# Kernel optimization log

Hardware: AMD Instinct MI355X
Metric: run time of the kernel (lower is better)

The kernel has to match this reference:

```python
import jax, jax.numpy as jnp
import numpy as np

NS, NV = 48, 10                    # scalar / vector multiplicities (cfg.ns, cfg.nv)
WN = NS * NS + NS * NV             # per-edge TP weight numel: paths 0e*0e->0e and 0e*1o->1o
OUT = NS + 3 * NV                  # out irreps 48x0e + 10x1o -> 78 dims
INV = float(1.0 / np.sqrt(NS))     # e3nn-style path normalization (fan_in = mul_in)
N_LIG, N_REC, N_ATOM = 2000, 2000, 15000
E_LL, E_RR, E_AA = 15000, 10000, 15000
E_LR, E_LA, E_AR = 5000, 8000, 8000


def setup_inputs() -> dict:
    key = jax.random.key(0)
    ks = jax.random.split(key, 40)
    f = lambda i, shape, s=1.0: jax.random.normal(ks[i], shape, dtype=jnp.float32) * s
    ii = lambda i, n, e: jax.random.randint(ks[i], (e,), 0, n, dtype=jnp.int32)
    w_s = (1.0 / (3 * NS)) ** 0.5
    return {
        'lig_x': f(0, (N_LIG, NS)), 'rec_x': f(1, (N_REC, NS)), 'atom_x': f(2, (N_ATOM, NS)),
        'll_attr': f(3, (E_LL, NS)), 'rr_attr': f(4, (E_RR, NS)), 'aa_attr': f(5, (E_AA, NS)),
        'lr_attr': f(6, (E_LR, NS)), 'la_attr': f(7, (E_LA, NS)), 'ar_attr': f(8, (E_AR, NS)),
        'll_sh': f(9, (E_LL, 9)), 'rr_sh': f(10, (E_RR, 9)), 'aa_sh': f(11, (E_AA, 9)),
        'lr_sh': f(12, (E_LR, 9)), 'la_sh': f(13, (E_LA, 9)), 'ar_sh': f(14, (E_AR, 9)),
        'mlp_w1': f(15, (9, 3 * NS, 3 * NS), w_s), 'mlp_b1': jnp.zeros((9, 3 * NS), jnp.float32),
        'mlp_w2': f(16, (9, 3 * NS, 3 * NS), w_s), 'mlp_b2': jnp.zeros((9, 3 * NS), jnp.float32),
        'mlp_w3': f(17, (9, 3 * NS, WN), w_s), 'mlp_b3': jnp.zeros((9, WN), jnp.float32),
        'll_src': ii(18, N_LIG, E_LL), 'll_dst': ii(19, N_LIG, E_LL),
        'rr_src': ii(20, N_REC, E_RR), 'rr_dst': ii(21, N_REC, E_RR),
        'aa_src': ii(22, N_ATOM, E_AA), 'aa_dst': ii(23, N_ATOM, E_AA),
        'lr_lig': ii(24, N_LIG, E_LR), 'lr_rec': ii(25, N_REC, E_LR),
        'la_lig': ii(26, N_LIG, E_LA), 'la_atom': ii(27, N_ATOM, E_LA),
        'ar_atom': ii(28, N_ATOM, E_AR), 'ar_rec': ii(29, N_REC, E_AR),
    }


def _tp_conv(src_x, dst_x, e_attr, e_sh, src_idx, dst_idx, n_dst, w1, b1, w2, b2, w3, b3):
    """FullyConnectedTensorProductConv: per-edge MLP -> TP weights, CG tensor
    product of gathered source features with edge SH, mean scatter to dst."""
    fs = src_x[src_idx]                                          # (E, ns) gather
    z = jnp.concatenate([e_attr, fs, dst_x[dst_idx]], axis=-1)
    h = jax.nn.relu(z @ w1 + b1)
    h = jax.nn.relu(h @ w2 + b2)
    w = h @ w3 + b3                                              # (E, WN) edge-conditioned TP weights
    w0 = w[:, : NS * NS].reshape(-1, NS, NS)                     # 0e x 0e -> 0e path
    wv = w[:, NS * NS :].reshape(-1, NS, NV)                     # 0e x 1o -> 1o path
    out0 = jnp.einsum('ei,eio->eo', fs, w0) * e_sh[:, :1] * INV  # (E, ns)
    outv = jnp.einsum('ei,eiv,em->evm', fs, wv, e_sh[:, 1:4]) * INV  # (E, nv, 3)
    msg = jnp.concatenate([out0, outv.reshape(-1, NV * 3)], axis=-1)
    agg = jax.ops.segment_sum(msg, dst_idx, num_segments=n_dst)
    deg = jax.ops.segment_sum(jnp.ones((msg.shape[0], 1), msg.dtype), dst_idx, num_segments=n_dst)
    return agg / jnp.maximum(deg, 1.0)                           # mean reduction


def reference(lig_x, rec_x, atom_x, ll_attr, rr_attr, aa_attr, lr_attr, la_attr, ar_attr,
              ll_sh, rr_sh, aa_sh, lr_sh, la_sh, ar_sh,
              mlp_w1, mlp_b1, mlp_w2, mlp_b2, mlp_w3, mlp_b3,
              ll_src, ll_dst, rr_src, rr_dst, aa_src, aa_dst,
              lr_lig, lr_rec, la_lig, la_atom, ar_atom, ar_rec):
    P = lambda c: (mlp_w1[c], mlp_b1[c], mlp_w2[c], mlp_b2[c], mlp_w3[c], mlp_b3[c])
    # one interaction layer = 9 structurally distinct convs (lig/rec/atom intra + 6 cross dirs)
    lig_u = (_tp_conv(lig_x, lig_x, ll_attr, ll_sh, ll_src, ll_dst, N_LIG, *P(0))
           + _tp_conv(rec_x, lig_x, lr_attr, lr_sh, lr_rec, lr_lig, N_LIG, *P(1))
           + _tp_conv(atom_x, lig_x, la_attr, la_sh, la_atom, la_lig, N_LIG, *P(2)))
    rec_u = (_tp_conv(lig_x, rec_x, lr_attr, lr_sh, lr_lig, lr_rec, N_REC, *P(3))
           + _tp_conv(rec_x, rec_x, rr_attr, rr_sh, rr_src, rr_dst, N_REC, *P(4))
           + _tp_conv(atom_x, rec_x, ar_attr, ar_sh, ar_atom, ar_rec, N_REC, *P(5)))
    atom_u = (_tp_conv(lig_x, atom_x, la_attr, la_sh, la_lig, la_atom, N_ATOM, *P(6))
            + _tp_conv(rec_x, atom_x, ar_attr, ar_sh, ar_rec, ar_atom, N_ATOM, *P(7))
            + _tp_conv(atom_x, atom_x, aa_attr, aa_sh, aa_src, aa_dst, N_ATOM, *P(8)))
    pad = lambda x: jnp.pad(x, ((0, 0), (0, OUT - NS)))          # residual: pad scalars to out irreps
    return jnp.concatenate([pad(lig_x) + lig_u, pad(rec_x) + rec_u, pad(atom_x) + atom_u], axis=0)
```

## Files before the change

kernel.cpp:

```cpp
#include <hip/hip_runtime.h>


namespace {

constexpr int NCONV = 9;
constexpr int ETOT  = 82000;
constexpr float INV = 0.14433756729740643f;

constexpr int EC[NCONV]     = {15000,5000,8000,5000,10000,8000,8000,8000,15000};
constexpr int NBLKC[NCONV]  = {118,40,63,40,79,63,63,63,118};
constexpr int EOFF[NCONV]   = {0,15000,20000,28000,33000,43000,51000,59000,67000};
constexpr int DEGOFF[NCONV] = {0,2000,4000,6000,8000,10000,12000,27000,42000};
constexpr int NODEC[NCONV]  = {2000,2000,2000,2000,2000,2000,15000,15000,15000};
constexpr int NBLK_TOT = 647;

typedef _Float16 f16;
typedef __attribute__((ext_vector_type(8))) _Float16 f16x8;
typedef __attribute__((ext_vector_type(4))) _Float16 f16x4;
typedef __attribute__((ext_vector_type(4))) float f32x4;

#define MFMA(a, b, c) __builtin_amdgcn_mfma_f32_16x16x32_f16((a), (b), (c), 0, 0, 0)

struct ConvPtrs {
  const float* src_x[NCONV];
  const float* dst_x[NCONV];
  const float* attr[NCONV];
  const float* sh[NCONV];
  const int*   sidx[NCONV];
  const int*   didx[NCONV];
};

}

__device__ __forceinline__ int xcd_remap(int bid) {
  const int xcd = bid & 7, slot = bid >> 3;
  return (xcd <= 6) ? (xcd * 81 + slot) : (567 + slot);
}

__device__ __forceinline__ int conv_decode(int bid, int& rem) {
  int c = 0; rem = bid;
  while (c < NCONV - 1 && rem >= NBLKC[c]) { rem -= NBLKC[c]; ++c; }
  return c;
}

__device__ __forceinline__ void gld_lds16(const void* g, void* l) {
  __builtin_amdgcn_global_load_lds(
      (const __attribute__((address_space(1))) void*)g,
      (__attribute__((address_space(3))) void*)l, 16, 0, 0);
}

__device__ __forceinline__ f32x4 cvt4(f16x4 h) {
  return (f32x4){(float)h[0], (float)h[1], (float)h[2], (float)h[3]};
}

__global__ __launch_bounds__(64) void prep_w12(
    const float* __restrict__ w1, const float* __restrict__ b1,
    const float* __restrict__ w2, const float* __restrict__ b2,
    f16* __restrict__ w1f, f16* __restrict__ w2f) {
  const int b = blockIdx.x;
  const int sel = b >= 405, bb = sel ? b - 405 : b;
  const int c = bb / 45, r2 = bb % 45, cb = r2 / 5, s = r2 % 5;
  const float* w  = sel ? w2 : w1;
  const float* bi = sel ? b2 : b1;
  f16* dst = (sel ? w2f : w1f) + ((size_t)(c * 9 + cb) * 5 + s) * 512;
  const int l = threadIdx.x;
  const int n = cb * 16 + (l & 15);
  f16x8 pack;
#pragma unroll
  for (int j = 0; j < 8; ++j) {
    const int k = s * 32 + ((l >> 4) << 3) + j;
    float v = 0.f;
    if (k < 144)       v = w[((size_t)c * 144 + k) * 144 + n];
    else if (k == 144) v = bi[c * 144 + n];
    pack[j] = (f16)v;
  }
  ((f16x8*)dst)[l] = pack;
}

__global__ __launch_bounds__(256) void prep_w3k(
    const float* __restrict__ w3, const float* __restrict__ b3,
    f16* __restrict__ w3f) {
  const int b = blockIdx.x;
  const int c = b / 48, i = b % 48;
  const float* wc = w3 + (size_t)c * 144 * 2784;
  const float* bc = b3 + (size_t)c * 2784;
  f16* dst = w3f + (size_t)(c * 48 + i) * 20 * 512;
#pragma unroll 1
  for (int it = 0; it < 40; ++it) {
    const int f = it * 256 + threadIdx.x;
    const int s = f >> 11, g2 = f & 2047, cb = g2 >> 9, l = (g2 >> 3) & 63, j = f & 7;
    const int k = s * 32 + ((l >> 4) << 3) + j;
    const int col = cb * 16 + (l & 15);
    float v = 0.f;
    if (k <= 144) {
      const float* src = (k == 144) ? bc : (wc + (size_t)k * 2784);
      if (col < 48)      v = src[i * 48 + col];
      else if (col < 58) v = src[2304 + i * 10 + (col - 48)];
    }
    dst[f] = (f16)v;
  }
}

__global__ __launch_bounds__(256) void deg_kernel(ConvPtrs P, float* __restrict__ deg) {
  const int gid = blockIdx.x * 256 + threadIdx.x;
  if (gid >= ETOT) return;
  int c = 0;
  while (c < NCONV - 1 && gid >= EOFF[c + 1]) ++c;
  const int e = gid - EOFF[c];
  atomicAdd(&deg[DEGOFF[c] + P.didx[c][e]], 1.0f);
}

__global__ __launch_bounds__(256) void scan_kernel(
    const float* __restrict__ deg, int* __restrict__ offs, int* __restrict__ cursor) {
  __shared__ int part[256];
  const int c = blockIdx.x, N = NODEC[c], base = DEGOFF[c];
  const int tid = threadIdx.x;
  const int chunk = (N + 255) / 256;
  const int start = tid * chunk;
  const int end = (start + chunk < N) ? (start + chunk) : N;
  int s = 0;
  for (int i = start; i < end; ++i) s += (int)deg[base + i];
  part[tid] = s;
  __syncthreads();
  if (tid == 0) {
    int acc = 0;
    for (int k = 0; k < 256; ++k) { int t = part[k]; part[k] = acc; acc += t; }
  }
  __syncthreads();
  int acc = part[tid];
  for (int i = start; i < end; ++i) {
    offs[base + i] = acc; cursor[base + i] = acc;
    acc += (int)deg[base + i];
  }
}

__global__ __launch_bounds__(256) void slot_kernel(
    ConvPtrs P, int* __restrict__ cursor, int* __restrict__ eslot) {
  const int gid = blockIdx.x * 256 + threadIdx.x;
  if (gid >= ETOT) return;
  int c = 0;
  while (c < NCONV - 1 && gid >= EOFF[c + 1]) ++c;
  const int e = gid - EOFF[c];
  const int d = P.didx[c][e];
  const int pos = atomicAdd(&cursor[DEGOFF[c] + d], 1);
  eslot[EOFF[c] + pos] = e;
}

template<int NCB, int CB0>
__device__ __forceinline__ void layer_mm(
    const f16x8* __restrict__ Av, const f16x8* __restrict__ wv,
    int c, int lane, int wr, f32x4 acc[4][5]) {
#pragma unroll
  for (int rb = 0; rb < 4; ++rb)
#pragma unroll
    for (int cb = 0; cb < NCB; ++cb) acc[rb][cb] = (f32x4)0.0f;
#pragma unroll
  for (int s = 0; s < 5; ++s) {
    f16x8 B[NCB];
#pragma unroll
    for (int cb = 0; cb < NCB; ++cb)
      B[cb] = wv[((size_t)(c * 9 + CB0 + cb) * 5 + s) * 64 + lane];
    f16x8 A[4];
#pragma unroll
    for (int rb = 0; rb < 4; ++rb) A[rb] = Av[((wr * 4 + rb) * 5 + s) * 64 + lane];
#pragma unroll
    for (int rb = 0; rb < 4; ++rb)
#pragma unroll
      for (int cb = 0; cb < NCB; ++cb)
        acc[rb][cb] = MFMA(A[rb], B[cb], acc[rb][cb]);
  }
}

template<int NCB, int CB0>
__device__ __forceinline__ void layer_wb(const f32x4 acc[4][5], f16* __restrict__ At,
                                         int lane, int wr) {
#pragma unroll
  for (int cb = 0; cb < NCB; ++cb) {
    const int k = (CB0 + cb) * 16 + (lane & 15);
    const int s = k >> 5, g = (k >> 3) & 3, j = k & 7;
#pragma unroll
    for (int rb = 0; rb < 4; ++rb)
#pragma unroll
      for (int r = 0; r < 4; ++r) {
        const int row = ((lane >> 4) << 2) + r;
        At[((((wr * 4 + rb) * 5 + s) * 4 + g) * 16 + row) * 8 + j] =
            (f16)fmaxf(acc[rb][cb][r], 0.f);
      }
  }
}

__global__ __launch_bounds__(256, 3) void fused_conv(
    ConvPtrs P, const f16* __restrict__ w1f, const f16* __restrict__ w2f,
    const f16* __restrict__ w3f, float* __restrict__ medge) {
  __shared__ __align__(16) char smem[54272];
  f16* Atile = (f16*)smem;
  f16 (*fst)[128] = (f16 (*)[128])(smem + 40960);
  int* sidb = (int*)(smem + 53248);
  int* dstb = (int*)(smem + 53760);

  int rem; const int c = conv_decode(xcd_remap(blockIdx.x), rem);
  const int E = EC[c], e0 = rem * 128;
  const int tid = threadIdx.x, lane = tid & 63, w = tid >> 6;
  const int wr = w >> 1, wc = w & 1;

  if (tid < 128) {
    int ec = e0 + tid; if (ec >= E) ec = E - 1;
    sidb[tid] = P.sidx[c][ec];
    dstb[tid] = P.didx[c][ec];
  }
  __syncthreads();

  {
    const float* attr = P.attr[c];
    const float* sx = P.src_x[c];
    const float* dx = P.dst_x[c];
#pragma unroll 1
    for (int it = 0; it < 10; ++it) {
      const int u = it * 256 + tid, j8 = u >> 7, e = u & 127;
      int ec = e0 + e; if (ec >= E) ec = E - 1;
      float v[8];
      if (j8 < 6) {
        const float* p = attr + (size_t)ec * 48 + j8 * 8;
#pragma unroll
        for (int t = 0; t < 8; ++t) v[t] = p[t];
      } else if (j8 < 12) {
        const float* p = sx + (size_t)sidb[e] * 48 + (j8 - 6) * 8;
#pragma unroll
        for (int t = 0; t < 8; ++t) v[t] = p[t];
#pragma unroll
        for (int t = 0; t < 8; ++t) fst[(j8 - 6) * 8 + t][e] = (f16)v[t];
      } else if (j8 < 18) {
        const float* p = dx + (size_t)dstb[e] * 48 + (j8 - 12) * 8;
#pragma unroll
        for (int t = 0; t < 8; ++t) v[t] = p[t];
      } else if (j8 == 18) {
        v[0] = 1.f;
#pragma unroll
        for (int t = 1; t < 8; ++t) v[t] = 0.f;
      } else {
#pragma unroll
        for (int t = 0; t < 8; ++t) v[t] = 0.f;
      }
      f16x8 h;
#pragma unroll
      for (int t = 0; t < 8; ++t) h[t] = (f16)v[t];
      const int s = j8 >> 2, g = j8 & 3, rbg = e >> 4, row = e & 15;
      ((f16x8*)Atile)[((rbg * 5 + s) * 4 + g) * 16 + row] = h;
    }
  }
  __syncthreads();

  const f16x8* Av = (const f16x8*)Atile;

  f32x4 acc[4][5];
  if (wc == 0) layer_mm<5, 0>(Av, (const f16x8*)w1f, c, lane, wr, acc);
  else         layer_mm<4, 5>(Av, (const f16x8*)w1f, c, lane, wr, acc);
  __syncthreads();
  if (wc == 0) layer_wb<5, 0>(acc, Atile, lane, wr);
  else         layer_wb<4, 5>(acc, Atile, lane, wr);
  __syncthreads();
  if (wc == 0) layer_mm<5, 0>(Av, (const f16x8*)w2f, c, lane, wr, acc);
  else         layer_mm<4, 5>(Av, (const f16x8*)w2f, c, lane, wr, acc);
  __syncthreads();
  if (wc == 0) layer_wb<5, 0>(acc, Atile, lane, wr);
  else         layer_wb<4, 5>(acc, Atile, lane, wr);
  __syncthreads();

  f16x8 Af[4][5];
#pragma unroll
  for (int rb = 0; rb < 4; ++rb)
#pragma unroll
    for (int s = 0; s < 5; ++s)
      Af[rb][s] = Av[((wr * 4 + rb) * 5 + s) * 64 + lane];
  __syncthreads();

  const f16* __restrict__ w3c = w3f + (size_t)(c * 48) * 10240;
  f16* buf0 = Atile;
  f16* buf1 = Atile + 10240;

  f32x4 msg[4][2];
#pragma unroll
  for (int rb = 0; rb < 4; ++rb)
#pragma unroll
    for (int cb = 0; cb < 2; ++cb) msg[rb][cb] = (f32x4)0.0f;

#pragma unroll
  for (int q = 0; q < 5; ++q) {
    const int chunk = q * 4 + w;
    gld_lds16(w3c + chunk * 512 + lane * 8, buf0 + chunk * 512);
  }
  __syncthreads();

#pragma unroll 1
  for (int i = 0; i < 48; ++i) {
    f16* bcur = (i & 1) ? buf1 : buf0;
    f16* bnxt = (i & 1) ? buf0 : buf1;
    if (i + 1 < 48) {
      const f16* gsrc = w3c + (size_t)(i + 1) * 10240;
#pragma unroll
      for (int q = 0; q < 5; ++q) {
        const int chunk = q * 4 + w;
        gld_lds16(gsrc + chunk * 512 + lane * 8, bnxt + chunk * 512);
      }
    }
    f16x4 fsh[4];
#pragma unroll
    for (int rb = 0; rb < 4; ++rb)
      fsh[rb] = *(const f16x4*)&fst[i][wr * 64 + rb * 16 + ((lane >> 4) << 2)];

    const f16x8* bv = (const f16x8*)bcur;
#pragma unroll
    for (int cb = 0; cb < 2; ++cb) {
      f16x8 Bf[5];
#pragma unroll
      for (int s = 0; s < 5; ++s) Bf[s] = bv[(s * 4 + wc * 2 + cb) * 64 + lane];
      f32x4 T[4];
#pragma unroll
      for (int rb = 0; rb < 4; ++rb) T[rb] = (f32x4)0.0f;
#pragma unroll
      for (int s = 0; s < 5; ++s)
#pragma unroll
        for (int rb = 0; rb < 4; ++rb) T[rb] = MFMA(Af[rb][s], Bf[s], T[rb]);
#pragma unroll
      for (int rb = 0; rb < 4; ++rb) msg[rb][cb] += cvt4(fsh[rb]) * T[rb];
    }
    __syncthreads();
  }

  const float* __restrict__ shp = P.sh[c];
#pragma unroll
  for (int rb = 0; rb < 4; ++rb)
#pragma unroll
    for (int r = 0; r < 4; ++r) {
      const int el = wr * 64 + rb * 16 + ((lane >> 4) << 2) + r;
      const int ec = e0 + el;
      if (ec >= E) continue;
      const size_t ge = (size_t)(EOFF[c] + ec);
      const float* shq = shp + (size_t)ec * 9;
      const float s0 = shq[0], s1 = shq[1], s2 = shq[2], s3 = shq[3];
      float* mp = medge + ge * 80;
#pragma unroll
      for (int cb = 0; cb < 2; ++cb) {
        const int col = (wc * 2 + cb) * 16 + (lane & 15);
        const float v = msg[rb][cb][r] * INV;
        if (col < 48) {
          mp[col] = v * s0;
        } else if (col < 58) {
          const int vv = col - 48;
          mp[48 + vv * 3 + 0] = v * s1;
          mp[48 + vv * 3 + 1] = v * s2;
          mp[48 + vv * 3 + 2] = v * s3;
        }
      }
    }
}

__global__ __launch_bounds__(256) void finalize_kernel(
    const float* __restrict__ lig, const float* __restrict__ rec,
    const float* __restrict__ atom, const float* __restrict__ deg,
    const int* __restrict__ offs, const int* __restrict__ eslot,
    const float* __restrict__ medge, float* __restrict__ out) {
  const int half = threadIdx.x >> 7;
  const int j = threadIdx.x & 127;
  const int row = blockIdx.x * 2 + half;
  if (row >= 19000 || j >= 78) return;
  int node, cb; const float* x;
  if (row < 2000)      { node = row;        cb = 0; x = lig; }
  else if (row < 4000) { node = row - 2000; cb = 3; x = rec; }
  else                 { node = row - 4000; cb = 6; x = atom; }
  float r = (j < 48) ? x[(size_t)node * 48 + j] : 0.f;
#pragma unroll
  for (int t = 0; t < 3; ++t) {
    const int c = cb + t;
    const int base = DEGOFF[c] + node;
    const float d = deg[base];
    const int n = (int)d;
    const int o = offs[base];
    float s = 0.f;
    for (int k = 0; k < n; ++k) {
      const int e = eslot[EOFF[c] + o + k];
      s += medge[(size_t)(EOFF[c] + e) * 80 + j];
    }
    r += s * (1.f / fmaxf(d, 1.f));
  }
  out[(size_t)row * 78 + j] = r;
}

extern "C" void kernel_launch(void* const* d_in, const int* in_sizes, int n_in,
                              void* d_out, int out_size, void* d_ws, size_t ws_size,
                              hipStream_t stream) {
  (void)in_sizes; (void)n_in; (void)out_size; (void)ws_size;
  const float* lig_x  = (const float*)d_in[0];
  const float* rec_x  = (const float*)d_in[1];
  const float* atom_x = (const float*)d_in[2];
  const float* attr_ll = (const float*)d_in[3];
  const float* attr_rr = (const float*)d_in[4];
  const float* attr_aa = (const float*)d_in[5];
  const float* attr_lr = (const float*)d_in[6];
  const float* attr_la = (const float*)d_in[7];
  const float* attr_ar = (const float*)d_in[8];
  const float* sh_ll = (const float*)d_in[9];
  const float* sh_rr = (const float*)d_in[10];
  const float* sh_aa = (const float*)d_in[11];
  const float* sh_lr = (const float*)d_in[12];
  const float* sh_la = (const float*)d_in[13];
  const float* sh_ar = (const float*)d_in[14];
  const float* w1 = (const float*)d_in[15];
  const float* b1 = (const float*)d_in[16];
  const float* w2 = (const float*)d_in[17];
  const float* b2 = (const float*)d_in[18];
  const float* w3 = (const float*)d_in[19];
  const float* b3 = (const float*)d_in[20];
  const int* ll_src = (const int*)d_in[21];
  const int* ll_dst = (const int*)d_in[22];
  const int* rr_src = (const int*)d_in[23];
  const int* rr_dst = (const int*)d_in[24];
  const int* aa_src = (const int*)d_in[25];
  const int* aa_dst = (const int*)d_in[26];
  const int* lr_lig = (const int*)d_in[27];
  const int* lr_rec = (const int*)d_in[28];
  const int* la_lig = (const int*)d_in[29];
  const int* la_atom = (const int*)d_in[30];
  const int* ar_atom = (const int*)d_in[31];
  const int* ar_rec  = (const int*)d_in[32];

  f16* w1f = (f16*)d_ws;
  f16* w2f = w1f + 207360;
  f16* w3f = w2f + 207360;
  float* deg   = (float*)(w3f + 4423680);
  int*   offs  = (int*)(deg + 57000);
  int*   cursor= offs + 57000;
  int*   eslot = cursor + 57000;
  float* medge = (float*)(eslot + 82000);

  ConvPtrs P;
  const float* SX[NCONV] = {lig_x, rec_x, atom_x, lig_x, rec_x, atom_x, lig_x, rec_x, atom_x};
  const float* DX[NCONV] = {lig_x, lig_x, lig_x, rec_x, rec_x, rec_x, atom_x, atom_x, atom_x};
  const float* AT[NCONV] = {attr_ll, attr_lr, attr_la, attr_lr, attr_rr, attr_ar, attr_la, attr_ar, attr_aa};
  const float* SH[NCONV] = {sh_ll, sh_lr, sh_la, sh_lr, sh_rr, sh_ar, sh_la, sh_ar, sh_aa};
  const int*   SI[NCONV] = {ll_src, lr_rec, la_atom, lr_lig, rr_src, ar_atom, la_lig, ar_rec, aa_src};
  const int*   DI[NCONV] = {ll_dst, lr_lig, la_lig, lr_rec, rr_dst, ar_rec, la_atom, ar_atom, aa_dst};
  for (int cc = 0; cc < NCONV; ++cc) {
    P.src_x[cc] = SX[cc]; P.dst_x[cc] = DX[cc]; P.attr[cc] = AT[cc];
    P.sh[cc] = SH[cc]; P.sidx[cc] = SI[cc]; P.didx[cc] = DI[cc];
  }

  prep_w12<<<810, 64, 0, stream>>>(w1, b1, w2, b2, w1f, w2f);
  prep_w3k<<<432, 256, 0, stream>>>(w3, b3, w3f);
  hipMemsetAsync(deg, 0, 57000 * sizeof(float), stream);
  deg_kernel<<<(ETOT + 255) / 256, 256, 0, stream>>>(P, deg);
  scan_kernel<<<NCONV, 256, 0, stream>>>(deg, offs, cursor);
  slot_kernel<<<(ETOT + 255) / 256, 256, 0, stream>>>(P, cursor, eslot);
  fused_conv<<<NBLK_TOT, 256, 0, stream>>>(P, w1f, w2f, w3f, medge);
  finalize_kernel<<<9500, 256, 0, stream>>>(lig_x, rec_x, atom_x, deg, offs,
                                            eslot, medge, (float*)d_out);
}
```

Baseline: 231.9 us.

## Write edge messages in CSR slot order and merge prep kernels

The three weight-prep kernels and the degree count are merged into one launch. The slot kernel now records each edge's CSR position, and fused_conv writes pre-scaled messages (including the 1/deg mean) straight into that sorted slot. Finalize then reads each node's messages as one contiguous range with no indirection, and each block handles 3 rows of 80 threads. This removes the eslot gather and one launch, at the cost of scattered writes in fused_conv and a deg lookup per edge.

```diff
diff --git a/kernel.cpp b/kernel.cpp
--- a/kernel.cpp
+++ b/kernel.cpp
@@ -53,61 +53,62 @@
   return (f32x4){(float)h[0], (float)h[1], (float)h[2], (float)h[3]};
 }
 
-__global__ __launch_bounds__(64) void prep_w12(
+__global__ __launch_bounds__(256) void prep_all(
+    ConvPtrs P,
     const float* __restrict__ w1, const float* __restrict__ b1,
     const float* __restrict__ w2, const float* __restrict__ b2,
-    f16* __restrict__ w1f, f16* __restrict__ w2f) {
-  const int b = blockIdx.x;
-  const int sel = b >= 405, bb = sel ? b - 405 : b;
-  const int c = bb / 45, r2 = bb % 45, cb = r2 / 5, s = r2 % 5;
-  const float* w  = sel ? w2 : w1;
-  const float* bi = sel ? b2 : b1;
-  f16* dst = (sel ? w2f : w1f) + ((size_t)(c * 9 + cb) * 5 + s) * 512;
-  const int l = threadIdx.x;
-  const int n = cb * 16 + (l & 15);
-  f16x8 pack;
-#pragma unroll
-  for (int j = 0; j < 8; ++j) {
-    const int k = s * 32 + ((l >> 4) << 3) + j;
-    float v = 0.f;
-    if (k < 144)       v = w[((size_t)c * 144 + k) * 144 + n];
-    else if (k == 144) v = bi[c * 144 + n];
-    pack[j] = (f16)v;
-  }
-  ((f16x8*)dst)[l] = pack;
-}
-
-__global__ __launch_bounds__(256) void prep_w3k(
     const float* __restrict__ w3, const float* __restrict__ b3,
-    f16* __restrict__ w3f) {
-  const int b = blockIdx.x;
-  const int c = b / 48, i = b % 48;
-  const float* wc = w3 + (size_t)c * 144 * 2784;
-  const float* bc = b3 + (size_t)c * 2784;
-  f16* dst = w3f + (size_t)(c * 48 + i) * 20 * 512;
+    f16* __restrict__ w1f, f16* __restrict__ w2f, f16* __restrict__ w3f,
+    float* __restrict__ deg) {
+  const int blk = blockIdx.x;
+  if (blk < 203) {
+    const int unit = blk * 4 + (threadIdx.x >> 6);
+    if (unit >= 810) return;
+    const int l = threadIdx.x & 63;
+    const int sel = unit >= 405, bb = sel ? unit - 405 : unit;
+    const int c = bb / 45, r2 = bb % 45, cb = r2 / 5, s = r2 % 5;
+    const float* w  = sel ? w2 : w1;
+    const float* bi = sel ? b2 : b1;
+    f16* dst = (sel ? w2f : w1f) + ((size_t)(c * 9 + cb) * 5 + s) * 512;
+    const int n = cb * 16 + (l & 15);
+    f16x8 pack;
+#pragma unroll
+    for (int j = 0; j < 8; ++j) {
+      const int k = s * 32 + ((l >> 4) << 3) + j;
+      float v = 0.f;
+      if (k < 144)       v = w[((size_t)c * 144 + k) * 144 + n];
+      else if (k == 144) v = bi[c * 144 + n];
+      pack[j] = (f16)v;
+    }
+    ((f16x8*)dst)[l] = pack;
+  } else if (blk < 635) {
+    const int b = blk - 203;
+    const int c = b / 48, i = b % 48;
+    const float* wc = w3 + (size_t)c * 144 * 2784;
+    const float* bc = b3 + (size_t)c * 2784;
+    f16* dst = w3f + (size_t)(c * 48 + i) * 20 * 512;
 #pragma unroll 1
-  for (int it = 0; it < 40; ++it) {
-    const int f = it * 256 + threadIdx.x;
-    const int s = f >> 11, g2 = f & 2047, cb = g2 >> 9, l = (g2 >> 3) & 63, j = f & 7;
-    const int k = s * 32 + ((l >> 4) << 3) + j;
-    const int col = cb * 16 + (l & 15);
-    float v = 0.f;
-    if (k <= 144) {
-      const float* src = (k == 144) ? bc : (wc + (size_t)k * 2784);
-      if (col < 48)      v = src[i * 48 + col];
-      else if (col < 58) v = src[2304 + i * 10 + (col - 48)];
-    }
-    dst[f] = (f16)v;
-  }
-}
-
-__global__ __launch_bounds__(256) void deg_kernel(ConvPtrs P, float* __restrict__ deg) {
-  const int gid = blockIdx.x * 256 + threadIdx.x;
-  if (gid >= ETOT) return;
-  int c = 0;
-  while (c < NCONV - 1 && gid >= EOFF[c + 1]) ++c;
-  const int e = gid - EOFF[c];
-  atomicAdd(&deg[DEGOFF[c] + P.didx[c][e]], 1.0f);
+    for (int it = 0; it < 40; ++it) {
+      const int f = it * 256 + threadIdx.x;
+      const int s = f >> 11, g2 = f & 2047, cb = g2 >> 9, l = (g2 >> 3) & 63, j = f & 7;
+      const int k = s * 32 + ((l >> 4) << 3) + j;
+      const int col = cb * 16 + (l & 15);
+      float v = 0.f;
+      if (k <= 144) {
+        const float* src = (k == 144) ? bc : (wc + (size_t)k * 2784);
+        if (col < 48)      v = src[i * 48 + col];
+        else if (col < 58) v = src[2304 + i * 10 + (col - 48)];
+      }
+      dst[f] = (f16)v;
+    }
+  } else {
+    const int gid = (blk - 635) * 256 + threadIdx.x;
+    if (gid >= ETOT) return;
+    int c = 0;
+    while (c < NCONV - 1 && gid >= EOFF[c + 1]) ++c;
+    const int e = gid - EOFF[c];
+    atomicAdd(&deg[DEGOFF[c] + P.didx[c][e]], 1.0f);
+  }
 }
 
 __global__ __launch_bounds__(256) void scan_kernel(
@@ -135,15 +136,14 @@
 }
 
 __global__ __launch_bounds__(256) void slot_kernel(
-    ConvPtrs P, int* __restrict__ cursor, int* __restrict__ eslot) {
+    ConvPtrs P, int* __restrict__ cursor, int* __restrict__ inv_slot) {
   const int gid = blockIdx.x * 256 + threadIdx.x;
   if (gid >= ETOT) return;
   int c = 0;
   while (c < NCONV - 1 && gid >= EOFF[c + 1]) ++c;
   const int e = gid - EOFF[c];
   const int d = P.didx[c][e];
-  const int pos = atomicAdd(&cursor[DEGOFF[c] + d], 1);
-  eslot[EOFF[c] + pos] = e;
+  inv_slot[gid] = atomicAdd(&cursor[DEGOFF[c] + d], 1);
 }
 
 template<int NCB, int CB0>
@@ -191,7 +191,8 @@
 
 __global__ __launch_bounds__(256, 3) void fused_conv(
     ConvPtrs P, const f16* __restrict__ w1f, const f16* __restrict__ w2f,
-    const f16* __restrict__ w3f, float* __restrict__ medge) {
+    const f16* __restrict__ w3f, const float* __restrict__ deg,
+    const int* __restrict__ inv_slot, float* __restrict__ medge) {
   __shared__ __align__(16) char smem[54272];
   f16* Atile = (f16*)smem;
   f16 (*fst)[128] = (f16 (*)[128])(smem + 40960);
@@ -328,6 +329,7 @@
   }
 
   const float* __restrict__ shp = P.sh[c];
+  const float* __restrict__ degc = deg + DEGOFF[c];
 #pragma unroll
   for (int rb = 0; rb < 4; ++rb)
 #pragma unroll
@@ -335,14 +337,16 @@
       const int el = wr * 64 + rb * 16 + ((lane >> 4) << 2) + r;
       const int ec = e0 + el;
       if (ec >= E) continue;
-      const size_t ge = (size_t)(EOFF[c] + ec);
+      const int dst = dstb[el];
+      const float sc = INV / fmaxf(degc[dst], 1.f);
       const float* shq = shp + (size_t)ec * 9;
       const float s0 = shq[0], s1 = shq[1], s2 = shq[2], s3 = shq[3];
-      float* mp = medge + ge * 80;
+      const int pos = inv_slot[EOFF[c] + ec];
+      float* mp = medge + (size_t)(EOFF[c] + pos) * 80;
 #pragma unroll
       for (int cb = 0; cb < 2; ++cb) {
         const int col = (wc * 2 + cb) * 16 + (lane & 15);
-        const float v = msg[rb][cb][r] * INV;
+        const float v = msg[rb][cb][r] * sc;
         if (col < 48) {
           mp[col] = v * s0;
         } else if (col < 58) {
@@ -357,12 +361,13 @@
 
 __global__ __launch_bounds__(256) void finalize_kernel(
     const float* __restrict__ lig, const float* __restrict__ rec,
-    const float* __restrict__ atom, const float* __restrict__ deg,
-    const int* __restrict__ offs, const int* __restrict__ eslot,
-    const float* __restrict__ medge, float* __restrict__ out) {
-  const int half = threadIdx.x >> 7;
-  const int j = threadIdx.x & 127;
-  const int row = blockIdx.x * 2 + half;
+    const float* __restrict__ atom, const int* __restrict__ offs,
+    const int* __restrict__ cursor, const float* __restrict__ medge,
+    float* __restrict__ out) {
+  const int tid = threadIdx.x;
+  if (tid >= 240) return;
+  const int r3 = tid / 80, j = tid - r3 * 80;
+  const int row = blockIdx.x * 3 + r3;
   if (row >= 19000 || j >= 78) return;
   int node, cb; const float* x;
   if (row < 2000)      { node = row;        cb = 0; x = lig; }
@@ -373,15 +378,9 @@
   for (int t = 0; t < 3; ++t) {
     const int c = cb + t;
     const int base = DEGOFF[c] + node;
-    const float d = deg[base];
-    const int n = (int)d;
-    const int o = offs[base];
-    float s = 0.f;
-    for (int k = 0; k < n; ++k) {
-      const int e = eslot[EOFF[c] + o + k];
-      s += medge[(size_t)(EOFF[c] + e) * 80 + j];
-    }
-    r += s * (1.f / fmaxf(d, 1.f));
+    const int o = offs[base], e = cursor[base];
+    for (int k = o; k < e; ++k)
+      r += medge[(size_t)(EOFF[c] + k) * 80 + j];
   }
   out[(size_t)row * 78 + j] = r;
 }
@@ -427,11 +426,11 @@
   f16* w1f = (f16*)d_ws;
   f16* w2f = w1f + 207360;
   f16* w3f = w2f + 207360;
-  float* deg   = (float*)(w3f + 4423680);
-  int*   offs  = (int*)(deg + 57000);
-  int*   cursor= offs + 57000;
-  int*   eslot = cursor + 57000;
-  float* medge = (float*)(eslot + 82000);
+  float* deg     = (float*)(w3f + 4423680);
+  int*   offs    = (int*)(deg + 57000);
+  int*   cursor  = offs + 57000;
+  int*   inv_slot= cursor + 57000;
+  float* medge   = (float*)(inv_slot + 82000);
 
   ConvPtrs P;
   const float* SX[NCONV] = {lig_x, rec_x, atom_x, lig_x, rec_x, atom_x, lig_x, rec_x, atom_x};
@@ -445,13 +444,11 @@
     P.sh[cc] = SH[cc]; P.sidx[cc] = SI[cc]; P.didx[cc] = DI[cc];
   }
 
-  prep_w12<<<810, 64, 0, stream>>>(w1, b1, w2, b2, w1f, w2f);
-  prep_w3k<<<432, 256, 0, stream>>>(w3, b3, w3f);
   hipMemsetAsync(deg, 0, 57000 * sizeof(float), stream);
-  deg_kernel<<<(ETOT + 255) / 256, 256, 0, stream>>>(P, deg);
+  prep_all<<<956, 256, 0, stream>>>(P, w1, b1, w2, b2, w3, b3, w1f, w2f, w3f, deg);
   scan_kernel<<<NCONV, 256, 0, stream>>>(deg, offs, cursor);
-  slot_kernel<<<(ETOT + 255) / 256, 256, 0, stream>>>(P, cursor, eslot);
-  fused_conv<<<NBLK_TOT, 256, 0, stream>>>(P, w1f, w2f, w3f, medge);
-  finalize_kernel<<<9500, 256, 0, stream>>>(lig_x, rec_x, atom_x, deg, offs,
-                                            eslot, medge, (float*)d_out);
-}
+  slot_kernel<<<(ETOT + 255) / 256, 256, 0, stream>>>(P, cursor, inv_slot);
+  fused_conv<<<NBLK_TOT, 256, 0, stream>>>(P, w1f, w2f, w3f, deg, inv_slot, medge);
+  finalize_kernel<<<(19000 + 2) / 3, 256, 0, stream>>>(lig_x, rec_x, atom_x, offs,
+                                                       cursor, medge, (float*)d_out);
+}
```

Measured after the change: 216.2 us. 6.8% less time.
